# Kernel optimization log

Measured on AMD Instinct MI355X. Metric: run time of the kernel, lower is better.

The kernel has to match this reference:

```python
import jax, jax.numpy as jnp
import numpy as np

EPS = 1e-3  # BN1d eps from norm_cfg


def _vfe_layer(x, W, gamma, beta, max_out, cat_max):
    """x: (N, M, Cin); W: (Cout, Cin) torch Linear layout; BN in training mode
    (batch stats over voxels N and points M per channel), then ReLU."""
    y = jnp.einsum('nmc,oc->nmo', x, W)            # (N, M, Cout)
    mean = y.mean(axis=(0, 1))                     # (Cout,)
    var = y.var(axis=(0, 1))                       # biased var, as BN uses
    y = (y - mean) * jax.lax.rsqrt(var + EPS) * gamma + beta
    pointwise = jax.nn.relu(y)                     # (N, M, Cout)
    if not max_out:
        return pointwise
    aggregated = pointwise.max(axis=1, keepdims=True)  # (N, 1, Cout)
    if not cat_max:
        return aggregated[:, 0, :]                 # (N, Cout)
    M = x.shape[1]
    repeated = jnp.broadcast_to(aggregated, (x.shape[0], M, aggregated.shape[2]))
    return jnp.concatenate([pointwise, repeated], axis=2)  # (N, M, 2*Cout)


def setup_inputs() -> dict:
    key = jax.random.key(0)
    ks = jax.random.split(key, 3)
    N, M, C = 20000, 64, 10
    return {
        'voxel_feats': jax.random.normal(ks[0], (N, M, C), dtype=jnp.float32),
        'W0': jax.random.normal(ks[1], (64, C), dtype=jnp.float32) * (1.0 / np.sqrt(C)),
        'gamma0': jnp.ones((64,), dtype=jnp.float32),
        'beta0': jnp.zeros((64,), dtype=jnp.float32),
        'W1': jax.random.normal(ks[2], (128, 128), dtype=jnp.float32) * (1.0 / np.sqrt(128)),
        'gamma1': jnp.ones((128,), dtype=jnp.float32),
        'beta1': jnp.zeros((128,), dtype=jnp.float32),
    }


def reference(voxel_feats, W0, gamma0, beta0, W1, gamma1, beta1):
    # layer 0: in=10 -> out=64, max_out=True, cat_max=True -> (N, M, 128)
    x = _vfe_layer(voxel_feats, W0, gamma0, beta0, max_out=True, cat_max=True)
    # layer 1 (last): in=128 -> out=128, max_out=True, cat_max=False -> (N, 128)
    x = _vfe_layer(x, W1, gamma1, beta1, max_out=True, cat_max=False)
    return x
```

## Files before the change

kernel.cpp:

```cpp
#include <hip/hip_runtime.h>

#define NVOX 20000
#define MPTS 64
#define CIN  10
#define NM   (NVOX*MPTS)
#define EPSBN 1e-3f

#define WS_SCALE0 0
#define WS_SHIFT0 64
#define WS_SCALE1 128
#define WS_SHIFT1 256

#define NB0   512
#define P0STR 72
#define NB1   2000
#define NBF   2000

typedef short bf16x8 __attribute__((ext_vector_type(8)));
typedef float f32x4  __attribute__((ext_vector_type(4)));
typedef unsigned int u32x4 __attribute__((ext_vector_type(4)));

__device__ __forceinline__ unsigned short f2bf(float f) {
    union { float f; unsigned u; } v; v.f = f;
    unsigned r = v.u + 0x7FFFu + ((v.u >> 16) & 1u);
    return (unsigned short)(r >> 16);
}
__device__ __forceinline__ unsigned cvtpk(float lo, float hi) {
    unsigned d;
    asm("v_cvt_pk_bf16_f32 %0, %1, %2" : "=v"(d) : "v"(lo), "v"(hi));
    return d;
}
__device__ __forceinline__ unsigned pkmax(unsigned a, unsigned b) {
    unsigned d;
    asm("v_pk_max_u16 %0, %1, %2" : "=v"(d) : "v"(a), "v"(b));
    return d;
}

__global__ __launch_bounds__(256) void k_stats0(const float* __restrict__ x,
                                                float* __restrict__ p0) {
    __shared__ float sm[4][P0STR];
    float sx[CIN];
    float sxx[55];
#pragma unroll
    for (int i = 0; i < CIN; i++) sx[i] = 0.f;
#pragma unroll
    for (int k = 0; k < 55; k++) sxx[k] = 0.f;

    const int t = threadIdx.x;
    const int tid = blockIdx.x * 256 + t;

    for (int g = tid; g < NM / 2; g += NB0 * 256) {
        const float4* xp = (const float4*)(x + (size_t)g * 20);
        float4 a = xp[0], b = xp[1], c = xp[2], d = xp[3], e = xp[4];
        float v0[CIN] = {a.x, a.y, a.z, a.w, b.x, b.y, b.z, b.w, c.x, c.y};
        float v1[CIN] = {c.z, c.w, d.x, d.y, d.z, d.w, e.x, e.y, e.z, e.w};
#pragma unroll
        for (int i = 0; i < CIN; i++) sx[i] += v0[i] + v1[i];
#pragma unroll
        for (int i = 0; i < CIN; i++)
#pragma unroll
            for (int j = 0; j <= i; j++)
                sxx[i * (i + 1) / 2 + j] += v0[i] * v0[j] + v1[i] * v1[j];
    }

    const int l = t & 63, w = t >> 6;
#pragma unroll
    for (int i = 0; i < CIN; i++) {
        float v = sx[i];
#pragma unroll
        for (int off = 32; off; off >>= 1) v += __shfl_xor(v, off, 64);
        if (l == 0) sm[w][i] = v;
    }
#pragma unroll
    for (int k = 0; k < 55; k++) {
        float v = sxx[k];
#pragma unroll
        for (int off = 32; off; off >>= 1) v += __shfl_xor(v, off, 64);
        if (l == 0) sm[w][10 + k] = v;
    }
    __syncthreads();
    if (t < 65)
        p0[blockIdx.x * P0STR + t] = sm[0][t] + sm[1][t] + sm[2][t] + sm[3][t];
}

__global__ void k_finalize0(const float* __restrict__ p0, float* __restrict__ ws,
                            const float* __restrict__ w0,
                            const float* __restrict__ gamma0, const float* __restrict__ beta0) {
    __shared__ float s[P0STR];
    const int t = threadIdx.x;
    if (t < 65) {
        float acc = 0.f;
#pragma unroll 8
        for (int r = 0; r < NB0; r++) acc += p0[r * P0STR + t];
        s[t] = acc;
    }
    __syncthreads();
    if (t < 64) {
        float w[CIN];
#pragma unroll
        for (int i = 0; i < CIN; i++) w[i] = w0[t * CIN + i];
        float m = 0.f;
#pragma unroll
        for (int i = 0; i < CIN; i++) m += w[i] * s[i];
        m *= (1.f / NM);
        float q = 0.f;
#pragma unroll
        for (int i = 0; i < CIN; i++)
#pragma unroll
            for (int j = 0; j <= i; j++)
                q += ((i == j) ? 1.f : 2.f) * w[i] * w[j] * s[10 + i * (i + 1) / 2 + j];
        q *= (1.f / NM);
        float var = q - m * m;
        float scale = gamma0[t] * rsqrtf(var + EPSBN);
        ws[WS_SCALE0 + t] = scale;
        ws[WS_SHIFT0 + t] = beta0[t] - m * scale;
    }
}

__global__ void k_finalize1(const float* __restrict__ p1, float* __restrict__ ws,
                            const float* __restrict__ gamma1, const float* __restrict__ beta1) {
    __shared__ float sm[2][4];
    const int c = blockIdx.x;
    const int t = threadIdx.x, l = t & 63, w = t >> 6;
    float s = 0.f, qq = 0.f;
    for (int r = t; r < NB1; r += 256) {
        s  += p1[(size_t)r * 256 + c];
        qq += p1[(size_t)r * 256 + 128 + c];
    }
#pragma unroll
    for (int off = 32; off; off >>= 1) { s += __shfl_xor(s, off, 64); qq += __shfl_xor(qq, off, 64); }
    if (l == 0) { sm[0][w] = s; sm[1][w] = qq; }
    __syncthreads();
    if (t == 0) {
        float S = sm[0][0] + sm[0][1] + sm[0][2] + sm[0][3];
        float Q = sm[1][0] + sm[1][1] + sm[1][2] + sm[1][3];
        float m = S * (1.f / NM);
        float var = Q * (1.f / NM) - m * m;
        float scale = gamma1[c] * rsqrtf(var + EPSBN);
        ws[WS_SCALE1 + c] = scale;
        ws[WS_SHIFT1 + c] = beta1[c] - m * scale;
    }
}

template <bool STATS>
__global__ __launch_bounds__(256) void k_pass(const float* __restrict__ x,
                                              const float* __restrict__ w0,
                                              const float* __restrict__ w1,
                                              const float* __restrict__ ws,
                                              float* __restrict__ pout) {
    __shared__ unsigned short xB[MPTS * 40];
    __shared__ unsigned short zB[MPTS * 72];
    __shared__ unsigned short aggP[4 * 64];
    __shared__ float pbuf[256];

    const int t  = threadIdx.x;
    const int l  = t & 63;
    const int w  = t >> 6;
    const int lr = l & 15;
    const int lg = l >> 4;

    for (int i = t; i < MPTS * 40 / 2; i += 256) ((unsigned*)xB)[i] = 0u;
    __syncthreads();
    if (t < 64) xB[t * 40 + 10] = 0x3F80;

    bf16x8 w0f[4];
#pragma unroll
    for (int mi = 0; mi < 4; mi++) {
        int ch = 16 * mi + lr;
        float sc = ws[WS_SCALE0 + ch], sh = ws[WS_SHIFT0 + ch];
        bf16x8 f;
#pragma unroll
        for (int j = 0; j < 8; j++) {
            int k = 8 * lg + j;
            float v = (k < CIN) ? sc * w0[ch * CIN + k] : (k == CIN ? sh : 0.f);
            f[j] = (short)f2bf(v);
        }
        w0f[mi] = f;
    }

    bf16x8 wfrag[2][4];
#pragma unroll
    for (int njl = 0; njl < 2; njl++) {
        const float* wrow = w1 + (32 * w + 16 * njl + lr) * 128;
#pragma unroll
        for (int ks = 0; ks < 4; ks++) {
            float4 a = *(const float4*)(wrow + 32 * ks + 8 * lg);
            float4 b = *(const float4*)(wrow + 32 * ks + 8 * lg + 4);
            bf16x8 f;
            f[0] = (short)f2bf(a.x); f[1] = (short)f2bf(a.y);
            f[2] = (short)f2bf(a.z); f[3] = (short)f2bf(a.w);
            f[4] = (short)f2bf(b.x); f[5] = (short)f2bf(b.y);
            f[6] = (short)f2bf(b.z); f[7] = (short)f2bf(b.w);
            wfrag[njl][ks] = f;
        }
    }

    float sc1[2], sh1[2];
    if (!STATS) {
#pragma unroll
        for (int njl = 0; njl < 2; njl++) {
            int col = 32 * w + 16 * njl + lr;
            sc1[njl] = ws[WS_SCALE1 + col];
            sh1[njl] = ws[WS_SHIFT1 + col];
        }
    }
    float as_[2] = {0.f, 0.f}, aq[2] = {0.f, 0.f};

    const int nblk = STATS ? NB1 : NBF;
    for (int n = blockIdx.x; n < NVOX; n += nblk) {
        if (t < 128) {
            int p = t >> 1, h = t & 1;
            const float* xp = x + (size_t)n * (MPTS * CIN) + p * CIN;
            if (h == 0) {
                float2 a = ((const float2*)xp)[0];
                float2 b = ((const float2*)xp)[1];
                uint2 d = { cvtpk(a.x, a.y), cvtpk(b.x, b.y) };
                *(uint2*)&xB[p * 40] = d;
            } else {
                float2 a = ((const float2*)(xp + 4))[0];
                float2 b = ((const float2*)(xp + 4))[1];
                float2 c = ((const float2*)(xp + 4))[2];
                uint2 d = { cvtpk(a.x, a.y), cvtpk(b.x, b.y) };
                *(uint2*)&xB[p * 40 + 4] = d;
                *(unsigned*)&xB[p * 40 + 8] = cvtpk(c.x, c.y);
            }
        }
        __syncthreads();

        {
            const int p = 16 * w + lr;
            bf16x8 bx = *(const bf16x8*)&xB[p * 40 + 8 * lg];
#pragma unroll
            for (int mi = 0; mi < 4; mi++) {
                f32x4 zz = {0.f, 0.f, 0.f, 0.f};
                f32x4 a0 = __builtin_amdgcn_mfma_f32_16x16x32_bf16(w0f[mi], bx, zz, 0, 0, 0);
                unsigned d0 = cvtpk(fmaxf(a0[0], 0.f), fmaxf(a0[1], 0.f));
                unsigned d1 = cvtpk(fmaxf(a0[2], 0.f), fmaxf(a0[3], 0.f));
                int chunk = 2 * mi + (lg >> 1);
                int idx = p * 72 + ((chunk ^ (p & 7)) << 3) + ((lg & 1) << 2);
                uint2 dd = {d0, d1};
                *(uint2*)&zB[idx] = dd;
            }
        }
        __syncthreads();

        {
            int cs = t & 7;
            int pa = (t >> 3) * 2, pb = pa + 1;
            u32x4 ra = *(const u32x4*)&zB[pa * 72 + ((cs ^ (pa & 7)) << 3)];
            u32x4 rb = *(const u32x4*)&zB[pb * 72 + ((cs ^ (pb & 7)) << 3)];
            u32x4 m;
#pragma unroll
            for (int k2 = 0; k2 < 4; k2++) m[k2] = pkmax(ra[k2], rb[k2]);
#pragma unroll
            for (int off = 8; off <= 32; off <<= 1)
#pragma unroll
                for (int k2 = 0; k2 < 4; k2++) m[k2] = pkmax(m[k2], __shfl_xor(m[k2], off));
            if (l < 8) *(u32x4*)&aggP[w * 64 + l * 8] = m;
        }
        __syncthreads();

        bf16x8 bz[4][2];
#pragma unroll
        for (int pj = 0; pj < 4; pj++) {
            int p = 16 * pj + lr;
#pragma unroll
            for (int ks = 0; ks < 2; ks++)
                bz[pj][ks] = *(const bf16x8*)&zB[p * 72 + (((4 * ks + lg) ^ (p & 7)) << 3)];
        }
        bf16x8 gfrag[2];
#pragma unroll
        for (int ks = 0; ks < 2; ks++) {
            int sl = (4 * ks + lg) * 8;
            u32x4 g = *(const u32x4*)&aggP[sl];
#pragma unroll
            for (int wv = 1; wv < 4; wv++) {
                u32x4 h2 = *(const u32x4*)&aggP[wv * 64 + sl];
#pragma unroll
                for (int k2 = 0; k2 < 4; k2++) g[k2] = pkmax(g[k2], h2[k2]);
            }
            gfrag[ks] = __builtin_bit_cast(bf16x8, g);
        }

        f32x4 dacc[2];
#pragma unroll
        for (int njl = 0; njl < 2; njl++) {
            f32x4 zz = {0.f, 0.f, 0.f, 0.f};
            zz = __builtin_amdgcn_mfma_f32_16x16x32_bf16(gfrag[0], wfrag[njl][2], zz, 0, 0, 0);
            dacc[njl] = __builtin_amdgcn_mfma_f32_16x16x32_bf16(gfrag[1], wfrag[njl][3], zz, 0, 0, 0);
        }

        float vm[2] = {0.f, 0.f};
#pragma unroll
        for (int njl = 0; njl < 2; njl++) {
#pragma unroll
            for (int mi = 0; mi < 4; mi++) {
                f32x4 acc = dacc[njl];
                acc = __builtin_amdgcn_mfma_f32_16x16x32_bf16(bz[mi][0], wfrag[njl][0], acc, 0, 0, 0);
                acc = __builtin_amdgcn_mfma_f32_16x16x32_bf16(bz[mi][1], wfrag[njl][1], acc, 0, 0, 0);
                if (STATS) {
#pragma unroll
                    for (int r = 0; r < 4; r++) { as_[njl] += acc[r]; aq[njl] += acc[r] * acc[r]; }
                } else {
#pragma unroll
                    for (int r = 0; r < 4; r++)
                        vm[njl] = fmaxf(vm[njl], fmaxf(fmaf(acc[r], sc1[njl], sh1[njl]), 0.f));
                }
            }
        }

        if (!STATS) {
#pragma unroll
            for (int njl = 0; njl < 2; njl++) {
                float v = vm[njl];
                v = fmaxf(v, __shfl_xor(v, 16));
                v = fmaxf(v, __shfl_xor(v, 32));
                if (l < 16) pout[(size_t)n * 128 + 32 * w + 16 * njl + l] = v;
            }
        }
    }

    if (STATS) {
#pragma unroll
        for (int njl = 0; njl < 2; njl++) {
            float s = as_[njl];
            s += __shfl_xor(s, 16); s += __shfl_xor(s, 32);
            float qq = aq[njl];
            qq += __shfl_xor(qq, 16); qq += __shfl_xor(qq, 32);
            if (l < 16) {
                int col = 32 * w + 16 * njl + l;
                pbuf[col] = s;
                pbuf[128 + col] = qq;
            }
        }
        __syncthreads();
        pout[(size_t)blockIdx.x * 256 + t] = pbuf[t];
    }
}

extern "C" void kernel_launch(void* const* d_in, const int* in_sizes, int n_in,
                              void* d_out, int out_size, void* d_ws, size_t ws_size,
                              hipStream_t stream) {
    (void)in_sizes; (void)n_in; (void)out_size; (void)ws_size;
    const float* x      = (const float*)d_in[0];
    const float* W0     = (const float*)d_in[1];
    const float* gamma0 = (const float*)d_in[2];
    const float* beta0  = (const float*)d_in[3];
    const float* W1     = (const float*)d_in[4];
    const float* gamma1 = (const float*)d_in[5];
    const float* beta1  = (const float*)d_in[6];
    float* out = (float*)d_out;
    float* ws  = (float*)d_ws;

    k_stats0<<<NB0, 256, 0, stream>>>(x, out);
    k_finalize0<<<1, 256, 0, stream>>>(out, ws, W0, gamma0, beta0);
    k_pass<true><<<NB1, 256, 0, stream>>>(x, W0, W1, ws, out);
    k_finalize1<<<128, 256, 0, stream>>>(out, ws, gamma1, beta1);
    k_pass<false><<<NBF, 256, 0, stream>>>(x, W0, W1, ws, out);
}
```

Measured before the change: 242.8 us.

## Prefetch next voxel input into registers and restructure per-wave staging to cut barriers

Each wave now loads and converts its own 16 points' input rows, so the first two block barriers per voxel can be dropped. The next voxel's input is prefetched into registers while the current one is processed, hiding global-load latency. The XOR swizzle on the z buffer is removed because writes and reads are now wave-local. A barrier is added after the fragment reads to protect the shared buffers before the next iteration, and the unswizzled layout may add LDS bank conflicts.

```diff
diff --git a/kernel.cpp b/kernel.cpp
--- a/kernel.cpp
+++ b/kernel.cpp
@@ -158,6 +158,9 @@
     const int w  = t >> 6;
     const int lr = l & 15;
     const int lg = l >> 4;
+    const int srow = 16 * w + (l >> 2);
+    const int ssub = l & 3;
+    const int prow = 16 * w + lr;
 
     for (int i = t; i < MPTS * 40 / 2; i += 256) ((unsigned*)xB)[i] = 0u;
     __syncthreads();
@@ -206,49 +209,49 @@
     }
     float as_[2] = {0.f, 0.f}, aq[2] = {0.f, 0.f};
 
+    __syncthreads();
+
+    float2 pfa, pfb;
+    {
+        const float* xr = x + (size_t)blockIdx.x * 640 + srow * 10;
+        if (ssub < 2) { pfa = *(const float2*)(xr + ssub * 4); pfb = *(const float2*)(xr + ssub * 4 + 2); }
+        else if (ssub == 2) { pfa = *(const float2*)(xr + 8); }
+    }
+
     const int nblk = STATS ? NB1 : NBF;
     for (int n = blockIdx.x; n < NVOX; n += nblk) {
-        if (t < 128) {
-            int p = t >> 1, h = t & 1;
-            const float* xp = x + (size_t)n * (MPTS * CIN) + p * CIN;
-            if (h == 0) {
-                float2 a = ((const float2*)xp)[0];
-                float2 b = ((const float2*)xp)[1];
-                uint2 d = { cvtpk(a.x, a.y), cvtpk(b.x, b.y) };
-                *(uint2*)&xB[p * 40] = d;
-            } else {
-                float2 a = ((const float2*)(xp + 4))[0];
-                float2 b = ((const float2*)(xp + 4))[1];
-                float2 c = ((const float2*)(xp + 4))[2];
-                uint2 d = { cvtpk(a.x, a.y), cvtpk(b.x, b.y) };
-                *(uint2*)&xB[p * 40 + 4] = d;
-                *(unsigned*)&xB[p * 40 + 8] = cvtpk(c.x, c.y);
-            }
-        }
-        __syncthreads();
-
+        if (ssub < 2) {
+            uint2 d = { cvtpk(pfa.x, pfa.y), cvtpk(pfb.x, pfb.y) };
+            *(uint2*)&xB[srow * 40 + ssub * 4] = d;
+        } else if (ssub == 2) {
+            *(unsigned*)&xB[srow * 40 + 8] = cvtpk(pfa.x, pfa.y);
+        }
         {
-            const int p = 16 * w + lr;
-            bf16x8 bx = *(const bf16x8*)&xB[p * 40 + 8 * lg];
+            int nn = n + nblk;
+            if (nn < NVOX) {
+                const float* xr = x + (size_t)nn * 640 + srow * 10;
+                if (ssub < 2) { pfa = *(const float2*)(xr + ssub * 4); pfb = *(const float2*)(xr + ssub * 4 + 2); }
+                else if (ssub == 2) { pfa = *(const float2*)(xr + 8); }
+            }
+        }
+
+        {
+            bf16x8 bx = *(const bf16x8*)&xB[prow * 40 + 8 * lg];
 #pragma unroll
             for (int mi = 0; mi < 4; mi++) {
                 f32x4 zz = {0.f, 0.f, 0.f, 0.f};
                 f32x4 a0 = __builtin_amdgcn_mfma_f32_16x16x32_bf16(w0f[mi], bx, zz, 0, 0, 0);
-                unsigned d0 = cvtpk(fmaxf(a0[0], 0.f), fmaxf(a0[1], 0.f));
-                unsigned d1 = cvtpk(fmaxf(a0[2], 0.f), fmaxf(a0[3], 0.f));
-                int chunk = 2 * mi + (lg >> 1);
-                int idx = p * 72 + ((chunk ^ (p & 7)) << 3) + ((lg & 1) << 2);
-                uint2 dd = {d0, d1};
-                *(uint2*)&zB[idx] = dd;
-            }
-        }
-        __syncthreads();
+                uint2 dd = { cvtpk(fmaxf(a0[0], 0.f), fmaxf(a0[1], 0.f)),
+                             cvtpk(fmaxf(a0[2], 0.f), fmaxf(a0[3], 0.f)) };
+                *(uint2*)&zB[prow * 72 + 16 * mi + 4 * lg] = dd;
+            }
+        }
 
         {
-            int cs = t & 7;
-            int pa = (t >> 3) * 2, pb = pa + 1;
-            u32x4 ra = *(const u32x4*)&zB[pa * 72 + ((cs ^ (pa & 7)) << 3)];
-            u32x4 rb = *(const u32x4*)&zB[pb * 72 + ((cs ^ (pb & 7)) << 3)];
+            int cs = l & 7;
+            int pa = 16 * w + 2 * (l >> 3);
+            u32x4 ra = *(const u32x4*)&zB[pa * 72 + cs * 8];
+            u32x4 rb = *(const u32x4*)&zB[(pa + 1) * 72 + cs * 8];
             u32x4 m;
 #pragma unroll
             for (int k2 = 0; k2 < 4; k2++) m[k2] = pkmax(ra[k2], rb[k2]);
@@ -258,7 +261,9 @@
                 for (int k2 = 0; k2 < 4; k2++) m[k2] = pkmax(m[k2], __shfl_xor(m[k2], off));
             if (l < 8) *(u32x4*)&aggP[w * 64 + l * 8] = m;
         }
-        __syncthreads();
+
+        asm volatile("s_waitcnt lgkmcnt(0)" ::: "memory");
+        __builtin_amdgcn_s_barrier();
 
         bf16x8 bz[4][2];
 #pragma unroll
@@ -266,7 +271,7 @@
             int p = 16 * pj + lr;
 #pragma unroll
             for (int ks = 0; ks < 2; ks++)
-                bz[pj][ks] = *(const bf16x8*)&zB[p * 72 + (((4 * ks + lg) ^ (p & 7)) << 3)];
+                bz[pj][ks] = *(const bf16x8*)&zB[p * 72 + (4 * ks + lg) * 8];
         }
         bf16x8 gfrag[2];
 #pragma unroll
@@ -281,6 +286,9 @@
             }
             gfrag[ks] = __builtin_bit_cast(bf16x8, g);
         }
+
+        asm volatile("s_waitcnt lgkmcnt(0)" ::: "memory");
+        __builtin_amdgcn_s_barrier();
 
         f32x4 dacc[2];
 #pragma unroll
```

After: 220.9 us. 1.1x faster.
